# Kernel optimization log

Hardware: AMD Instinct MI355X
Metric: run time of the kernel (lower is better)

Reference implementation:

```python
import jax, jax.numpy as jnp
import numpy as np

NUM_HEADS = 32
NUM_KV_HEADS = 8
HEAD_DIM = 128
SCALE = 1.0 / float(np.sqrt(HEAD_DIM))
MAX_SEQLEN = 1024  # all packed sequences padded to this length
NUM_SEQS = 4
NEG_INF = -1e10  # same masking constant as the Triton kernel


def setup_inputs() -> dict:
    key = jax.random.key(0)
    k1, k2, k3 = jax.random.split(key, 3)
    T = NUM_SEQS * MAX_SEQLEN
    q = jax.random.normal(k1, (T, NUM_HEADS, HEAD_DIM), dtype=jnp.float32)
    k = jax.random.normal(k2, (T, NUM_KV_HEADS, HEAD_DIM), dtype=jnp.float32)
    v = jax.random.normal(k3, (T, NUM_KV_HEADS, HEAD_DIM), dtype=jnp.float32)
    cu_seqlens = (jnp.arange(NUM_SEQS + 1, dtype=jnp.int32) * MAX_SEQLEN)
    return {"q": q, "k": k, "v": v, "cu_seqlens": cu_seqlens}


def _varlen_causal_attention(q, k, v, cu_seqlens):
    """Causal GQA flash attention over ragged packed sequences.

    q: [T, H, D]; k, v: [T, HKV, D]; cu_seqlens: [B+1] int32.
    Faithful to flash_attention_varlen_kernel: per-sequence causal softmax
    attention with KV-head sharing (Q_head // (H // HKV)).
    """
    T, H, D = q.shape
    HKV = k.shape[1]
    rep = H // HKV
    B = cu_seqlens.shape[0] - 1
    S = MAX_SEQLEN

    seq_lens = cu_seqlens[1:] - cu_seqlens[:-1]              # [B]
    pos = jnp.arange(S, dtype=jnp.int32)                     # [S]
    valid = pos[None, :] < seq_lens[:, None]                 # [B, S]
    idx = cu_seqlens[:-1][:, None] + pos[None, :]            # [B, S]
    idx = jnp.where(valid, idx, 0)

    # Pad packed tokens into dense [B, S, H, D]
    qp = q[idx]                                              # [B, S, H, D]
    kp = jnp.repeat(k[idx], rep, axis=2)                     # [B, S, H, D]
    vp = jnp.repeat(v[idx], rep, axis=2)                     # [B, S, H, D]

    scores = jnp.einsum('bqhd,bkhd->bhqk', qp, kp) * SCALE   # [B, H, S, S]
    causal = pos[:, None] >= pos[None, :]                    # [S, S]
    mask = valid[:, None, :, None] & valid[:, None, None, :] & causal[None, None]
    scores = jnp.where(mask, scores, NEG_INF)
    probs = jax.nn.softmax(scores, axis=-1)                  # [B, H, S, S]
    out = jnp.einsum('bhqk,bkhd->bqhd', probs, vp)           # [B, S, H, D]

    # Scatter back to packed layout [T, H, D]
    out = out * valid[..., None, None]
    o = jnp.zeros_like(q).at[idx.reshape(-1)].add(out.reshape(B * S, H, D))
    return o


def reference(q, k, v, cu_seqlens):
    return _varlen_causal_attention(q, k, v, cu_seqlens)
```

## Files before the change

kernel.cpp:

```cpp
#include <hip/hip_runtime.h>
#include <hip/hip_bf16.h>

#define H 32
#define HKV 8
#define DD 128
#define SMAX 1024
#define QBLK 32
#define KVBLK 64
#define NQB (SMAX / QBLK)
#define QSCALE 0.12751770f

typedef __attribute__((ext_vector_type(8))) short bf16x8;
typedef __attribute__((ext_vector_type(4))) short bf16x4;
typedef __attribute__((ext_vector_type(4))) float f32x4;
typedef __attribute__((ext_vector_type(4))) unsigned short u16x4;

__device__ inline unsigned short f2bf(float f) {
  unsigned u = __float_as_uint(f);
  unsigned r = 0x7fffu + ((u >> 16) & 1u);
  return (unsigned short)((u + r) >> 16);
}

__device__ inline int swz(int x) { return ((x ^ (x >> 3)) & 15) << 3; }

__global__ __launch_bounds__(256) void fa_kernel(
    const float* __restrict__ q, const float* __restrict__ k,
    const float* __restrict__ v, const int* __restrict__ cu,
    float* __restrict__ out, int inner_n) {
  const int bx = blockIdx.x;
  const int inner = bx % inner_n;
  const int qb = NQB - 1 - (bx / inner_n);
  const int b = inner / HKV;
  const int kvh = inner % HKV;

  const int seq_start = cu[b];
  const int seq_len = cu[b + 1] - seq_start;
  if (qb * QBLK >= seq_len) return;

  const int tid = threadIdx.x;
  const int lane = tid & 63;
  const int w = tid >> 6;
  const int lg = lane >> 4;
  const int lr = lane & 15;
  const int h = kvh * (H / HKV) + w;

  __shared__ __align__(16) char kbuf[2][KVBLK * DD * 2];
  __shared__ __align__(16) char vbuf[2][DD * KVBLK * 2];
  __shared__ __align__(16) char pbuf[4][QBLK * KVBLK * 2];

  const float* kbase = k + (size_t)seq_start * (HKV * DD) + kvh * DD;
  const float* vbase = v + (size_t)seq_start * (HKV * DD) + kvh * DD;

  float4 reg[8];
  const int srow = tid >> 3;

#define LOAD_T(BASE, T)                                                   \
  do {                                                                    \
    int rbase_ = (T)*KVBLK;                                               \
    _Pragma("unroll") for (int i = 0; i < 8; ++i) {                       \
      int f4_ = i * 256 + tid;                                            \
      int row_ = f4_ >> 5;                                                \
      int c4_ = f4_ & 31;                                                 \
      size_t off_ =                                                       \
          (size_t)min(rbase_ + row_, seq_len - 1) * (HKV * DD) + c4_ * 4; \
      reg[i] = *(const float4*)((BASE) + off_);                           \
    }                                                                     \
  } while (0)

#define STORE_K(BI)                                                       \
  do {                                                                    \
    char* kb_ = kbuf[BI];                                                 \
    _Pragma("unroll") for (int i = 0; i < 8; ++i) {                       \
      int f4_ = i * 256 + tid;                                            \
      int row_ = f4_ >> 5;                                                \
      int c4_ = f4_ & 31;                                                 \
      u16x4 hh_;                                                          \
      hh_[0] = f2bf(reg[i].x); hh_[1] = f2bf(reg[i].y);                   \
      hh_[2] = f2bf(reg[i].z); hh_[3] = f2bf(reg[i].w);                   \
      *(u16x4*)(kb_ + row_ * 256 + ((c4_ * 8) ^ swz(row_))) = hh_;        \
    }                                                                     \
  } while (0)

#define STORE_V(BI)                                                       \
  do {                                                                    \
    char* vb_ = vbuf[BI];                                                 \
    _Pragma("unroll") for (int i = 0; i < 8; ++i) {                       \
      int f4_ = i * 256 + tid;                                            \
      int row_ = f4_ >> 5;                                                \
      int c4_ = f4_ & 31;                                                 \
      unsigned short v0_ = f2bf(reg[i].x), v1_ = f2bf(reg[i].y);          \
      unsigned short v2_ = f2bf(reg[i].z), v3_ = f2bf(reg[i].w);          \
      int d0_ = 4 * c4_;                                                  \
      *(unsigned short*)(vb_ + (d0_ + 0) * 128 + ((row_ * 2) ^ swz(d0_ + 0))) = v0_; \
      *(unsigned short*)(vb_ + (d0_ + 1) * 128 + ((row_ * 2) ^ swz(d0_ + 1))) = v1_; \
      *(unsigned short*)(vb_ + (d0_ + 2) * 128 + ((row_ * 2) ^ swz(d0_ + 2))) = v2_; \
      *(unsigned short*)(vb_ + (d0_ + 3) * 128 + ((row_ * 2) ^ swz(d0_ + 3))) = v3_; \
    }                                                                     \
  } while (0)

  LOAD_T(kbase, 0);

  bf16x8 qf[2][4];
#pragma unroll
  for (int m = 0; m < 2; ++m) {
    int q_pos = qb * QBLK + m * 16 + lr;
    int q_tok = seq_start + min(q_pos, seq_len - 1);
    const float* qp = q + (size_t)q_tok * (H * DD) + h * DD;
#pragma unroll
    for (int ks = 0; ks < 4; ++ks) {
      int d0 = 8 * lg + 32 * ks;
      float4 x = *(const float4*)(qp + d0);
      float4 y = *(const float4*)(qp + d0 + 4);
      bf16x8 tq;
      tq[0] = (short)f2bf(x.x * QSCALE); tq[1] = (short)f2bf(x.y * QSCALE);
      tq[2] = (short)f2bf(x.z * QSCALE); tq[3] = (short)f2bf(x.w * QSCALE);
      tq[4] = (short)f2bf(y.x * QSCALE); tq[5] = (short)f2bf(y.y * QSCALE);
      tq[6] = (short)f2bf(y.z * QSCALE); tq[7] = (short)f2bf(y.w * QSCALE);
      qf[m][ks] = tq;
    }
  }

  f32x4 o[2][8];
#pragma unroll
  for (int m = 0; m < 2; ++m)
#pragma unroll
    for (int i = 0; i < 8; ++i) o[m][i] = (f32x4){0.f, 0.f, 0.f, 0.f};
  float m_run[2][4], l_run[2][4];
#pragma unroll
  for (int m = 0; m < 2; ++m)
#pragma unroll
    for (int r = 0; r < 4; ++r) { m_run[m][r] = -1e30f; l_run[m][r] = 0.f; }

  char* pw = pbuf[w];
  const int qmax = qb * QBLK + QBLK - 1;
  const int tmax = qmax >> 6;

  STORE_K(0);
  LOAD_T(vbase, 0);
  STORE_V(0);
  __syncthreads();

  for (int t = 0; t <= tmax; ++t) {
    const int cur = t & 1;
    const int nxt = cur ^ 1;
    const char* kb_ = kbuf[cur];
    const char* vb_ = vbuf[cur];

    if (t < tmax) LOAD_T(kbase, t + 1);
    __builtin_amdgcn_sched_barrier(0);

    f32x4 s[2][4];
    __builtin_amdgcn_s_setprio(1);
#pragma unroll
    for (int n = 0; n < 4; ++n) {
      if (t * 64 + n * 16 <= qmax) {
        int kcol = n * 16 + lr;
        int key = swz(kcol);
        bf16x8 kb4[4];
#pragma unroll
        for (int ks = 0; ks < 4; ++ks) {
          int a0 = kcol * 256 + ((16 * lg + 64 * ks) ^ key);
          bf16x4 lo = *(const bf16x4*)(kb_ + a0);
          bf16x4 hi = *(const bf16x4*)(kb_ + (a0 ^ 8));
          bf16x8 t8;
          t8[0] = lo[0]; t8[1] = lo[1]; t8[2] = lo[2]; t8[3] = lo[3];
          t8[4] = hi[0]; t8[5] = hi[1]; t8[6] = hi[2]; t8[7] = hi[3];
          kb4[ks] = t8;
        }
#pragma unroll
        for (int m = 0; m < 2; ++m) {
          f32x4 acc = {0.f, 0.f, 0.f, 0.f};
#pragma unroll
          for (int ks = 0; ks < 4; ++ks)
            acc = __builtin_amdgcn_mfma_f32_16x16x32_bf16(qf[m][ks], kb4[ks], acc, 0, 0, 0);
          s[m][n] = acc;
        }
      } else {
        s[0][n] = (f32x4){-2e30f, -2e30f, -2e30f, -2e30f};
        s[1][n] = s[0][n];
      }
    }
    __builtin_amdgcn_s_setprio(0);

    if (t < tmax) {
      STORE_K(nxt);
      LOAD_T(vbase, t + 1);
    }
    __builtin_amdgcn_sched_barrier(0);

    if (t == tmax) {
#pragma unroll
      for (int n = 0; n < 4; ++n) {
        int kv_pos = t * 64 + n * 16 + lr;
#pragma unroll
        for (int m = 0; m < 2; ++m) {
          int qrow = qb * QBLK + m * 16 + 4 * lg;
#pragma unroll
          for (int r = 0; r < 4; ++r)
            if (kv_pos > qrow + r) s[m][n][r] = -2e30f;
        }
      }
    }

#pragma unroll
    for (int m = 0; m < 2; ++m) {
      float mx[4];
#pragma unroll
      for (int r = 0; r < 4; ++r) {
        float v0 = fmaxf(fmaxf(s[m][0][r], s[m][1][r]), fmaxf(s[m][2][r], s[m][3][r]));
#pragma unroll
        for (int off = 1; off < 16; off <<= 1)
          v0 = fmaxf(v0, __shfl_xor(v0, off, 64));
        mx[r] = v0;
      }
      float need = mx[0] - m_run[m][0];
#pragma unroll
      for (int r = 1; r < 4; ++r) need = fmaxf(need, mx[r] - m_run[m][r]);
      if (!__all(need <= 10.0f)) {
#pragma unroll
        for (int r = 0; r < 4; ++r) {
          float mn = fmaxf(m_run[m][r], mx[r]);
          float corr = exp2f(m_run[m][r] - mn);
          m_run[m][r] = mn;
          l_run[m][r] *= corr;
#pragma unroll
          for (int dt = 0; dt < 8; ++dt) o[m][dt][r] *= corr;
        }
      }
      float rsum[4] = {0.f, 0.f, 0.f, 0.f};
#pragma unroll
      for (int n = 0; n < 4; ++n) {
#pragma unroll
        for (int r = 0; r < 4; ++r) {
          float p = exp2f(s[m][n][r] - m_run[m][r]);
          rsum[r] += p;
          int prow = m * 16 + 4 * lg + r;
          int pcol = n * 16 + lr;
          *(unsigned short*)(pw + prow * 128 + ((pcol * 2) ^ swz(prow))) = f2bf(p);
        }
      }
#pragma unroll
      for (int r = 0; r < 4; ++r) {
        float rs = rsum[r];
#pragma unroll
        for (int off = 1; off < 16; off <<= 1)
          rs += __shfl_xor(rs, off, 64);
        l_run[m][r] += rs;
      }
    }

    const int nks = (t * 64 + 32 <= qmax) ? 2 : 1;
    __builtin_amdgcn_s_setprio(1);
    for (int ks = 0; ks < nks; ++ks) {
      bf16x8 pa[2];
#pragma unroll
      for (int m = 0; m < 2; ++m) {
        int prow = m * 16 + lr;
        int a0 = prow * 128 + ((16 * lg + 64 * ks) ^ swz(prow));
        bf16x4 lo = *(const bf16x4*)(pw + a0);
        bf16x4 hi = *(const bf16x4*)(pw + (a0 ^ 8));
        bf16x8 t8;
        t8[0] = lo[0]; t8[1] = lo[1]; t8[2] = lo[2]; t8[3] = lo[3];
        t8[4] = hi[0]; t8[5] = hi[1]; t8[6] = hi[2]; t8[7] = hi[3];
        pa[m] = t8;
      }
#pragma unroll
      for (int dt = 0; dt < 8; ++dt) {
        int d = dt * 16 + lr;
        int a0 = d * 128 + ((16 * lg + 64 * ks) ^ swz(d));
        bf16x4 lo = *(const bf16x4*)(vb_ + a0);
        bf16x4 hi = *(const bf16x4*)(vb_ + (a0 ^ 8));
        bf16x8 vbf;
        vbf[0] = lo[0]; vbf[1] = lo[1]; vbf[2] = lo[2]; vbf[3] = lo[3];
        vbf[4] = hi[0]; vbf[5] = hi[1]; vbf[6] = hi[2]; vbf[7] = hi[3];
#pragma unroll
        for (int m = 0; m < 2; ++m)
          o[m][dt] = __builtin_amdgcn_mfma_f32_16x16x32_bf16(pa[m], vbf, o[m][dt], 0, 0, 0);
      }
    }
    __builtin_amdgcn_s_setprio(0);

    if (t < tmax) STORE_V(nxt);
    __syncthreads();
  }

#pragma unroll
  for (int m = 0; m < 2; ++m) {
#pragma unroll
    for (int r = 0; r < 4; ++r) {
      int qp_ = qb * QBLK + m * 16 + 4 * lg + r;
      if (qp_ < seq_len) {
        float inv_l = 1.0f / l_run[m][r];
        float* op = out + (size_t)(seq_start + qp_) * (H * DD) + h * DD + lr;
#pragma unroll
        for (int dt = 0; dt < 8; ++dt) op[dt * 16] = o[m][dt][r] * inv_l;
      }
    }
  }
#undef LOAD_T
#undef STORE_K
#undef STORE_V
}

extern "C" void kernel_launch(void* const* d_in, const int* in_sizes, int n_in,
                              void* d_out, int out_size, void* d_ws, size_t ws_size,
                              hipStream_t stream) {
  const float* q = (const float*)d_in[0];
  const float* k = (const float*)d_in[1];
  const float* v = (const float*)d_in[2];
  const int* cu = (const int*)d_in[3];
  float* out = (float*)d_out;
  const int B = in_sizes[3] - 1;
  const int inner_n = B * HKV;
  dim3 grid(NQB * inner_n);
  fa_kernel<<<grid, 256, 0, stream>>>(q, k, v, cu, out, inner_n);
}
```

Baseline: 290.4 us.

## Transpose QK^T MFMA so each lane owns a query row; use packed bf16 converts

Swaps the MFMA operand order for the score computation so each lane holds one query row across four key columns. Row max and sum then need only two cross-lane shuffles instead of four per register, the online-softmax state shrinks to one value per lane, and P is written to LDS as packed 8-byte stores. All float-to-bf16 conversions switch from manual bit rounding to the hardware v_cvt_pk_bf16_f32 instruction. The trade-off is extra shuffles to broadcast the correction and normalisation factors into the O accumulator layout, plus a changed causal-mask index mapping that must stay correct.

```diff
diff --git a/kernel.cpp b/kernel.cpp
--- a/kernel.cpp
+++ b/kernel.cpp
@@ -13,12 +13,13 @@
 typedef __attribute__((ext_vector_type(8))) short bf16x8;
 typedef __attribute__((ext_vector_type(4))) short bf16x4;
 typedef __attribute__((ext_vector_type(4))) float f32x4;
-typedef __attribute__((ext_vector_type(4))) unsigned short u16x4;
-
-__device__ inline unsigned short f2bf(float f) {
-  unsigned u = __float_as_uint(f);
-  unsigned r = 0x7fffu + ((u >> 16) & 1u);
-  return (unsigned short)((u + r) >> 16);
+typedef __attribute__((ext_vector_type(4))) unsigned int u32x4;
+typedef __attribute__((ext_vector_type(2))) unsigned int u32x2;
+
+__device__ inline unsigned cvt_pk_bf16(float a, float b) {
+  unsigned r;
+  asm("v_cvt_pk_bf16_f32 %0, %1, %2" : "=v"(r) : "v"(a), "v"(b));
+  return r;
 }
 
 __device__ inline int swz(int x) { return ((x ^ (x >> 3)) & 15) << 3; }
@@ -52,7 +53,6 @@
   const float* vbase = v + (size_t)seq_start * (HKV * DD) + kvh * DD;
 
   float4 reg[8];
-  const int srow = tid >> 3;
 
 #define LOAD_T(BASE, T)                                                   \
   do {                                                                    \
@@ -74,10 +74,10 @@
       int f4_ = i * 256 + tid;                                            \
       int row_ = f4_ >> 5;                                                \
       int c4_ = f4_ & 31;                                                 \
-      u16x4 hh_;                                                          \
-      hh_[0] = f2bf(reg[i].x); hh_[1] = f2bf(reg[i].y);                   \
-      hh_[2] = f2bf(reg[i].z); hh_[3] = f2bf(reg[i].w);                   \
-      *(u16x4*)(kb_ + row_ * 256 + ((c4_ * 8) ^ swz(row_))) = hh_;        \
+      u32x2 u_;                                                           \
+      u_[0] = cvt_pk_bf16(reg[i].x, reg[i].y);                            \
+      u_[1] = cvt_pk_bf16(reg[i].z, reg[i].w);                            \
+      *(u32x2*)(kb_ + row_ * 256 + ((c4_ * 8) ^ swz(row_))) = u_;         \
     }                                                                     \
   } while (0)
 
@@ -88,13 +88,13 @@
       int f4_ = i * 256 + tid;                                            \
       int row_ = f4_ >> 5;                                                \
       int c4_ = f4_ & 31;                                                 \
-      unsigned short v0_ = f2bf(reg[i].x), v1_ = f2bf(reg[i].y);          \
-      unsigned short v2_ = f2bf(reg[i].z), v3_ = f2bf(reg[i].w);          \
+      unsigned ab_ = cvt_pk_bf16(reg[i].x, reg[i].y);                     \
+      unsigned cd_ = cvt_pk_bf16(reg[i].z, reg[i].w);                     \
       int d0_ = 4 * c4_;                                                  \
-      *(unsigned short*)(vb_ + (d0_ + 0) * 128 + ((row_ * 2) ^ swz(d0_ + 0))) = v0_; \
-      *(unsigned short*)(vb_ + (d0_ + 1) * 128 + ((row_ * 2) ^ swz(d0_ + 1))) = v1_; \
-      *(unsigned short*)(vb_ + (d0_ + 2) * 128 + ((row_ * 2) ^ swz(d0_ + 2))) = v2_; \
-      *(unsigned short*)(vb_ + (d0_ + 3) * 128 + ((row_ * 2) ^ swz(d0_ + 3))) = v3_; \
+      *(unsigned short*)(vb_ + (d0_ + 0) * 128 + ((row_ * 2) ^ swz(d0_ + 0))) = (unsigned short)ab_;         \
+      *(unsigned short*)(vb_ + (d0_ + 1) * 128 + ((row_ * 2) ^ swz(d0_ + 1))) = (unsigned short)(ab_ >> 16); \
+      *(unsigned short*)(vb_ + (d0_ + 2) * 128 + ((row_ * 2) ^ swz(d0_ + 2))) = (unsigned short)cd_;         \
+      *(unsigned short*)(vb_ + (d0_ + 3) * 128 + ((row_ * 2) ^ swz(d0_ + 3))) = (unsigned short)(cd_ >> 16); \
     }                                                                     \
   } while (0)
 
@@ -111,12 +111,12 @@
       int d0 = 8 * lg + 32 * ks;
       float4 x = *(const float4*)(qp + d0);
       float4 y = *(const float4*)(qp + d0 + 4);
-      bf16x8 tq;
-      tq[0] = (short)f2bf(x.x * QSCALE); tq[1] = (short)f2bf(x.y * QSCALE);
-      tq[2] = (short)f2bf(x.z * QSCALE); tq[3] = (short)f2bf(x.w * QSCALE);
-      tq[4] = (short)f2bf(y.x * QSCALE); tq[5] = (short)f2bf(y.y * QSCALE);
-      tq[6] = (short)f2bf(y.z * QSCALE); tq[7] = (short)f2bf(y.w * QSCALE);
-      qf[m][ks] = tq;
+      u32x4 tq;
+      tq[0] = cvt_pk_bf16(x.x * QSCALE, x.y * QSCALE);
+      tq[1] = cvt_pk_bf16(x.z * QSCALE, x.w * QSCALE);
+      tq[2] = cvt_pk_bf16(y.x * QSCALE, y.y * QSCALE);
+      tq[3] = cvt_pk_bf16(y.z * QSCALE, y.w * QSCALE);
+      qf[m][ks] = __builtin_bit_cast(bf16x8, tq);
     }
   }
 
@@ -125,15 +125,14 @@
   for (int m = 0; m < 2; ++m)
 #pragma unroll
     for (int i = 0; i < 8; ++i) o[m][i] = (f32x4){0.f, 0.f, 0.f, 0.f};
-  float m_run[2][4], l_run[2][4];
-#pragma unroll
-  for (int m = 0; m < 2; ++m)
-#pragma unroll
-    for (int r = 0; r < 4; ++r) { m_run[m][r] = -1e30f; l_run[m][r] = 0.f; }
+  float m_run[2], l_run[2];
+#pragma unroll
+  for (int m = 0; m < 2; ++m) { m_run[m] = -1e30f; l_run[m] = 0.f; }
 
   char* pw = pbuf[w];
   const int qmax = qb * QBLK + QBLK - 1;
   const int tmax = qmax >> 6;
+  const int prow_key[2] = {swz(lr), swz(16 + lr)};
 
   STORE_K(0);
   LOAD_T(vbase, 0);
@@ -154,12 +153,12 @@
 #pragma unroll
     for (int n = 0; n < 4; ++n) {
       if (t * 64 + n * 16 <= qmax) {
-        int kcol = n * 16 + lr;
-        int key = swz(kcol);
+        int krow = n * 16 + lr;
+        int key = swz(krow);
         bf16x8 kb4[4];
 #pragma unroll
         for (int ks = 0; ks < 4; ++ks) {
-          int a0 = kcol * 256 + ((16 * lg + 64 * ks) ^ key);
+          int a0 = krow * 256 + ((16 * lg + 64 * ks) ^ key);
           bf16x4 lo = *(const bf16x4*)(kb_ + a0);
           bf16x4 hi = *(const bf16x4*)(kb_ + (a0 ^ 8));
           bf16x8 t8;
@@ -172,7 +171,7 @@
           f32x4 acc = {0.f, 0.f, 0.f, 0.f};
 #pragma unroll
           for (int ks = 0; ks < 4; ++ks)
-            acc = __builtin_amdgcn_mfma_f32_16x16x32_bf16(qf[m][ks], kb4[ks], acc, 0, 0, 0);
+            acc = __builtin_amdgcn_mfma_f32_16x16x32_bf16(kb4[ks], qf[m][ks], acc, 0, 0, 0);
           s[m][n] = acc;
         }
       } else {
@@ -191,62 +190,55 @@
     if (t == tmax) {
 #pragma unroll
       for (int n = 0; n < 4; ++n) {
-        int kv_pos = t * 64 + n * 16 + lr;
+        int kv_pos = t * 64 + n * 16 + 4 * lg;
 #pragma unroll
         for (int m = 0; m < 2; ++m) {
-          int qrow = qb * QBLK + m * 16 + 4 * lg;
+          int qrow = qb * QBLK + m * 16 + lr;
 #pragma unroll
           for (int r = 0; r < 4; ++r)
-            if (kv_pos > qrow + r) s[m][n][r] = -2e30f;
+            if (kv_pos + r > qrow) s[m][n][r] = -2e30f;
         }
       }
     }
 
 #pragma unroll
     for (int m = 0; m < 2; ++m) {
-      float mx[4];
-#pragma unroll
-      for (int r = 0; r < 4; ++r) {
-        float v0 = fmaxf(fmaxf(s[m][0][r], s[m][1][r]), fmaxf(s[m][2][r], s[m][3][r]));
-#pragma unroll
-        for (int off = 1; off < 16; off <<= 1)
-          v0 = fmaxf(v0, __shfl_xor(v0, off, 64));
-        mx[r] = v0;
-      }
-      float need = mx[0] - m_run[m][0];
-#pragma unroll
-      for (int r = 1; r < 4; ++r) need = fmaxf(need, mx[r] - m_run[m][r]);
-      if (!__all(need <= 10.0f)) {
-#pragma unroll
-        for (int r = 0; r < 4; ++r) {
-          float mn = fmaxf(m_run[m][r], mx[r]);
-          float corr = exp2f(m_run[m][r] - mn);
-          m_run[m][r] = mn;
-          l_run[m][r] *= corr;
-#pragma unroll
-          for (int dt = 0; dt < 8; ++dt) o[m][dt][r] *= corr;
-        }
-      }
-      float rsum[4] = {0.f, 0.f, 0.f, 0.f};
+      float mx = fmaxf(
+          fmaxf(fmaxf(fmaxf(s[m][0][0], s[m][0][1]), fmaxf(s[m][0][2], s[m][0][3])),
+                fmaxf(fmaxf(s[m][1][0], s[m][1][1]), fmaxf(s[m][1][2], s[m][1][3]))),
+          fmaxf(fmaxf(fmaxf(s[m][2][0], s[m][2][1]), fmaxf(s[m][2][2], s[m][2][3])),
+                fmaxf(fmaxf(s[m][3][0], s[m][3][1]), fmaxf(s[m][3][2], s[m][3][3]))));
+      mx = fmaxf(mx, __shfl_xor(mx, 16, 64));
+      mx = fmaxf(mx, __shfl_xor(mx, 32, 64));
+      if (!__all(mx - m_run[m] <= 10.0f)) {
+        float mn = fmaxf(m_run[m], mx);
+        float corr = exp2f(m_run[m] - mn);
+        m_run[m] = mn;
+        l_run[m] *= corr;
+        float cr[4];
+#pragma unroll
+        for (int r = 0; r < 4; ++r) cr[r] = __shfl(corr, 4 * lg + r, 64);
+#pragma unroll
+        for (int dt = 0; dt < 8; ++dt)
+#pragma unroll
+          for (int r = 0; r < 4; ++r) o[m][dt][r] *= cr[r];
+      }
+      float rsum = 0.f;
 #pragma unroll
       for (int n = 0; n < 4; ++n) {
-#pragma unroll
-        for (int r = 0; r < 4; ++r) {
-          float p = exp2f(s[m][n][r] - m_run[m][r]);
-          rsum[r] += p;
-          int prow = m * 16 + 4 * lg + r;
-          int pcol = n * 16 + lr;
-          *(unsigned short*)(pw + prow * 128 + ((pcol * 2) ^ swz(prow))) = f2bf(p);
-        }
-      }
-#pragma unroll
-      for (int r = 0; r < 4; ++r) {
-        float rs = rsum[r];
-#pragma unroll
-        for (int off = 1; off < 16; off <<= 1)
-          rs += __shfl_xor(rs, off, 64);
-        l_run[m][r] += rs;
-      }
+        float p0 = exp2f(s[m][n][0] - m_run[m]);
+        float p1 = exp2f(s[m][n][1] - m_run[m]);
+        float p2 = exp2f(s[m][n][2] - m_run[m]);
+        float p3 = exp2f(s[m][n][3] - m_run[m]);
+        rsum += (p0 + p1) + (p2 + p3);
+        u32x2 pk;
+        pk[0] = cvt_pk_bf16(p0, p1);
+        pk[1] = cvt_pk_bf16(p2, p3);
+        *(u32x2*)(pw + (m * 16 + lr) * 128 + ((32 * n + 8 * lg) ^ prow_key[m])) = pk;
+      }
+      rsum += __shfl_xor(rsum, 16, 64);
+      rsum += __shfl_xor(rsum, 32, 64);
+      l_run[m] += rsum;
     }
 
     const int nks = (t * 64 + 32 <= qmax) ? 2 : 1;
@@ -255,8 +247,7 @@
       bf16x8 pa[2];
 #pragma unroll
       for (int m = 0; m < 2; ++m) {
-        int prow = m * 16 + lr;
-        int a0 = prow * 128 + ((16 * lg + 64 * ks) ^ swz(prow));
+        int a0 = (m * 16 + lr) * 128 + ((16 * lg + 64 * ks) ^ prow_key[m]);
         bf16x4 lo = *(const bf16x4*)(pw + a0);
         bf16x4 hi = *(const bf16x4*)(pw + (a0 ^ 8));
         bf16x8 t8;
@@ -286,14 +277,16 @@
 
 #pragma unroll
   for (int m = 0; m < 2; ++m) {
+    float linv[4];
+#pragma unroll
+    for (int r = 0; r < 4; ++r) linv[r] = 1.0f / __shfl(l_run[m], 4 * lg + r, 64);
 #pragma unroll
     for (int r = 0; r < 4; ++r) {
       int qp_ = qb * QBLK + m * 16 + 4 * lg + r;
       if (qp_ < seq_len) {
-        float inv_l = 1.0f / l_run[m][r];
         float* op = out + (size_t)(seq_start + qp_) * (H * DD) + h * DD + lr;
 #pragma unroll
-        for (int dt = 0; dt < 8; ++dt) op[dt * 16] = o[m][dt][r] * inv_l;
+        for (int dt = 0; dt < 8; ++dt) op[dt * 16] = o[m][dt][r] * linv[r];
       }
     }
   }
```

New measurement: 252.1 us. 13.2% less time.
